# Kernel tuning notes

Hardware: AMD Instinct MI355X
Metric: run time of the kernel (lower is better)

## Reference

```python
import jax, jax.numpy as jnp
import numpy as np

B, S, H, NH = 4, 2048, 1024, 16
D = H // NH

def setup_inputs() -> dict:
    key = jax.random.key(0)
    ks = jax.random.split(key, 9)
    sc = 1.0 / np.sqrt(H)
    return {
        "x": jax.random.normal(ks[0], (B, S, H), jnp.float32),
        "Wq": jax.random.normal(ks[1], (H, H), jnp.float32) * sc,
        "bq": jax.random.normal(ks[2], (H,), jnp.float32) * 0.01,
        "Wk": jax.random.normal(ks[3], (H, H), jnp.float32) * sc,
        "bk": jax.random.normal(ks[4], (H,), jnp.float32) * 0.01,
        "Wv": jax.random.normal(ks[5], (H, H), jnp.float32) * sc,
        "bv": jax.random.normal(ks[6], (H,), jnp.float32) * 0.01,
        "Wo": jax.random.normal(ks[7], (H, H), jnp.float32) * sc,
        "bo": jax.random.normal(ks[8], (H,), jnp.float32) * 0.01,
    }

def reference(x, Wq, bq, Wk, bk, Wv, bv, Wo, bo):
    # torch Linear: y = x @ W.T + b
    def proj(x, W, b):
        # [B,S,H] -> [B,NH,S,D]
        y = jnp.einsum('bsh,oh->bso', x, W) + b
        return y.reshape(B, S, NH, D).transpose(0, 2, 1, 3)
    q = proj(x, Wq, bq)
    k = proj(x, Wk, bk)
    v = proj(x, Wv, bv)
    scores = jnp.einsum('bhqd,bhkd->bhqk', q, k) / jnp.sqrt(jnp.float32(D))
    p = jax.nn.softmax(scores, axis=-1)  # [B,NH,S,S]
    o = jnp.einsum('bhqk,bhkd->bhqd', p, v)  # dropout p=0 (eval)
    o = o.transpose(0, 2, 1, 3).reshape(B, S, H)
    return jnp.einsum('bsh,oh->bso', o, Wo) + bo
```

## Files before the change

### kernel.cpp

```cpp
#include <hip/hip_runtime.h>


#define DEV __device__ __forceinline__

typedef __bf16 bf16x8 __attribute__((ext_vector_type(8)));
typedef __bf16 bf16x4 __attribute__((ext_vector_type(4)));
typedef __bf16 bf16x2 __attribute__((ext_vector_type(2)));
typedef float floatx4 __attribute__((ext_vector_type(4)));
typedef unsigned int uintx4 __attribute__((ext_vector_type(4)));

constexpr int Bdim = 4, SS = 2048, HH = 1024, NHH = 16, DD = 64;
constexpr int MM = Bdim * SS;

DEV void async16(const void* g, void* l) {
  __builtin_amdgcn_global_load_lds(
      (const __attribute__((address_space(1))) unsigned int*)g,
      (__attribute__((address_space(3))) unsigned int*)l, 16, 0, 0);
}

DEV int swz2(int r) { return (r ^ (r >> 2)) & 3; }
DEV int swz3(int r) { return (r ^ (r >> 3)) & 7; }

DEV unsigned pkbf16(float lo, float hi) {
  bf16x2 t;
  t[0] = (__bf16)lo;
  t[1] = (__bf16)hi;
  return __builtin_bit_cast(unsigned, t);
}

DEV void pswap16(unsigned& a, unsigned& b) {
  asm("v_permlane16_swap_b32 %0, %1" : "+v"(a), "+v"(b));
}

__global__ __launch_bounds__(256) void cast_bf16_kernel(
    const float* __restrict__ x, const float* __restrict__ wq,
    const float* __restrict__ wk, const float* __restrict__ wv,
    const float* __restrict__ wo,
    __bf16* __restrict__ xb, __bf16* __restrict__ wqb, __bf16* __restrict__ wkb,
    __bf16* __restrict__ wvb, __bf16* __restrict__ wob) {
  const float* src; __bf16* dst; int n4;
  switch (blockIdx.z) {
    case 0: src = x;  dst = xb;  n4 = MM * HH / 4; break;
    case 1: src = wq; dst = wqb; n4 = HH * HH / 4; break;
    case 2: src = wk; dst = wkb; n4 = HH * HH / 4; break;
    case 3: src = wv; dst = wvb; n4 = HH * HH / 4; break;
    default: src = wo; dst = wob; n4 = HH * HH / 4; break;
  }
  int stride = gridDim.x * blockDim.x;
  for (int i = blockIdx.x * blockDim.x + threadIdx.x; i < n4; i += stride) {
    float4 v = ((const float4*)src)[i];
    bf16x4 o;
    o[0] = (__bf16)v.x; o[1] = (__bf16)v.y; o[2] = (__bf16)v.z; o[3] = (__bf16)v.w;
    ((bf16x4*)dst)[i] = o;
  }
}

__global__ __launch_bounds__(256, 3) void proj_qkv_kernel(
    const __bf16* __restrict__ xb,
    const __bf16* __restrict__ wqb, const __bf16* __restrict__ wkb,
    const __bf16* __restrict__ wvb,
    const float* __restrict__ bq, const float* __restrict__ bk,
    const float* __restrict__ bv,
    __bf16* __restrict__ Q, __bf16* __restrict__ Kc, __bf16* __restrict__ Vt) {
  __shared__ __align__(16) __bf16 As[2][128 * 32];
  __shared__ __align__(16) __bf16 Bs[2][3][64 * 32];

  const int lid = blockIdx.x;
  const int xcd = lid & 7, slot = lid >> 3;
  const int mp = xcd + 8 * (slot >> 4);
  const int np = slot & 15;
  const int m0 = mp * 128, n0 = np * 64;

  const int t = threadIdx.x;
  const int lane = t & 63, quad = lane >> 4, l16 = lane & 15;
  const int wid = t >> 6;

  const __bf16* const Wm[3] = {wqb, wkb, wvb};

  const int srow = t >> 2, sc = t & 3;
  const __bf16* Ag0 = xb + (size_t)(m0 + srow) * HH + (sc ^ swz2(srow)) * 8;
  const __bf16* Ag1 = xb + (size_t)(m0 + srow + 64) * HH + (sc ^ swz2(srow + 64)) * 8;
  const __bf16* Bg[3];
#pragma unroll
  for (int mo = 0; mo < 3; ++mo)
    Bg[mo] = Wm[mo] + (size_t)(n0 + srow) * HH + (sc ^ swz2(srow)) * 8;

  int aoff[2], boff[4];
#pragma unroll
  for (int mi = 0; mi < 2; ++mi) {
    int ra = wid * 32 + mi * 16 + l16;
    aoff[mi] = ra * 32 + (quad ^ swz2(ra)) * 8;
  }
#pragma unroll
  for (int ni = 0; ni < 4; ++ni) {
    int rb = ni * 16 + l16;
    boff[ni] = rb * 32 + (quad ^ swz2(rb)) * 8;
  }

  floatx4 acc[3][2][4] = {};

  async16(Ag0, &As[0][t * 8]);
  async16(Ag1, &As[0][2048 + t * 8]);
#pragma unroll
  for (int mo = 0; mo < 3; ++mo) async16(Bg[mo], &Bs[0][mo][t * 8]);

  for (int it = 0; it < HH / 32; ++it) {
    const int cur = it & 1;
    __syncthreads();

    if (it + 1 < HH / 32) {
      const int k = (it + 1) * 32;
      const int nxt = cur ^ 1;
      async16(Ag0 + k, &As[nxt][t * 8]);
      async16(Ag1 + k, &As[nxt][2048 + t * 8]);
#pragma unroll
      for (int mo = 0; mo < 3; ++mo) async16(Bg[mo] + k, &Bs[nxt][mo][t * 8]);
    }

    bf16x8 af[2];
#pragma unroll
    for (int mi = 0; mi < 2; ++mi) af[mi] = *(const bf16x8*)&As[cur][aoff[mi]];
#pragma unroll
    for (int mo = 0; mo < 3; ++mo) {
      bf16x8 bfr[4];
#pragma unroll
      for (int ni = 0; ni < 4; ++ni) bfr[ni] = *(const bf16x8*)&Bs[cur][mo][boff[ni]];
#pragma unroll
      for (int mi = 0; mi < 2; ++mi)
#pragma unroll
        for (int ni = 0; ni < 4; ++ni)
          acc[mo][mi][ni] = __builtin_amdgcn_mfma_f32_16x16x32_bf16(
              af[mi], bfr[ni], acc[mo][mi][ni], 0, 0, 0);
    }
  }

  const float qscale = 0.125f * 1.44269504088896f;
#pragma unroll
  for (int mo = 0; mo < 3; ++mo) {
    const float* bias = mo == 0 ? bq : mo == 1 ? bk : bv;
#pragma unroll
    for (int ni = 0; ni < 4; ++ni) {
      int n = n0 + ni * 16 + l16;
      float bval = bias[n];
      int h = n >> 6, d = n & 63;
#pragma unroll
      for (int mi = 0; mi < 2; ++mi) {
        int mbase = m0 + wid * 32 + mi * 16 + quad * 4;
        int bb = mbase >> 11, sbase = mbase & (SS - 1);
        size_t bh = (size_t)(bb * NHH + h);
        if (mo == 2) {
          bf16x4 pv;
#pragma unroll
          for (int r = 0; r < 4; ++r) pv[r] = (__bf16)(acc[mo][mi][ni][r] + bval);
          *(bf16x4*)&Vt[(bh * DD + d) * SS + sbase] = pv;
        } else {
#pragma unroll
          for (int r = 0; r < 4; ++r) {
            float v = acc[mo][mi][ni][r] + bval;
            if (mo == 0) Q [(bh * SS + sbase + r) * DD + d] = (__bf16)(v * qscale);
            else         Kc[(bh * SS + sbase + r) * DD + d] = (__bf16)v;
          }
        }
      }
    }
  }
}

DEV void gemm_db128(const __bf16* __restrict__ Ablk, const __bf16* __restrict__ Bblk,
                    __bf16* As, __bf16* Bs, floatx4 acc[4][4]) {
  const int t = threadIdx.x;
  const int lane = t & 63, quad = lane >> 4, l16 = lane & 15;
  const int wid = t >> 6;
  const int wm = (wid >> 1) * 64, wn = (wid & 1) * 64;

  const int srow = t >> 2, sc = t & 3;
  const __bf16* Ag0 = Ablk + (size_t)srow * HH + (sc ^ swz2(srow)) * 8;
  const __bf16* Ag1 = Ablk + (size_t)(srow + 64) * HH + (sc ^ swz2(srow + 64)) * 8;
  const __bf16* Bg0 = Bblk + (size_t)srow * HH + (sc ^ swz2(srow)) * 8;
  const __bf16* Bg1 = Bblk + (size_t)(srow + 64) * HH + (sc ^ swz2(srow + 64)) * 8;

  int aoff[4], boff[4];
#pragma unroll
  for (int i = 0; i < 4; ++i) {
    int ra = wm + i * 16 + l16;
    aoff[i] = ra * 32 + (quad ^ swz2(ra)) * 8;
    int rb = wn + i * 16 + l16;
    boff[i] = rb * 32 + (quad ^ swz2(rb)) * 8;
  }

  async16(Ag0, As + t * 8);
  async16(Ag1, As + 2048 + t * 8);
  async16(Bg0, Bs + t * 8);
  async16(Bg1, Bs + 2048 + t * 8);

  for (int it = 0; it < HH / 32; ++it) {
    const int cur = it & 1;
    __syncthreads();

    if (it + 1 < HH / 32) {
      const int k = (it + 1) * 32;
      const int nxt = (cur ^ 1) * 4096;
      async16(Ag0 + k, As + nxt + t * 8);
      async16(Ag1 + k, As + nxt + 2048 + t * 8);
      async16(Bg0 + k, Bs + nxt + t * 8);
      async16(Bg1 + k, Bs + nxt + 2048 + t * 8);
    }

    bf16x8 af[4], bfr[4];
#pragma unroll
    for (int i = 0; i < 4; ++i) {
      af[i]  = *(const bf16x8*)&As[cur * 4096 + aoff[i]];
      bfr[i] = *(const bf16x8*)&Bs[cur * 4096 + boff[i]];
    }
#pragma unroll
    for (int mi = 0; mi < 4; ++mi)
#pragma unroll
      for (int ni = 0; ni < 4; ++ni)
        acc[mi][ni] = __builtin_amdgcn_mfma_f32_16x16x32_bf16(af[mi], bfr[ni],
                                                              acc[mi][ni], 0, 0, 0);
  }
}

__global__ __launch_bounds__(256) void proj_out_kernel(
    const __bf16* __restrict__ Ob, const __bf16* __restrict__ wob,
    const float* __restrict__ bo, float* __restrict__ out) {
  __shared__ __align__(16) __bf16 As[2 * 128 * 32];
  __shared__ __align__(16) __bf16 Bs[2 * 128 * 32];
  const int lid = blockIdx.x;
  const int xcd = lid & 7, slot = lid >> 3;
  const int mp = xcd + 8 * (slot >> 3);
  const int np = slot & 7;
  const int m0 = mp * 128, n0 = np * 128;
  floatx4 acc[4][4] = {};
  gemm_db128(Ob + (size_t)m0 * HH, wob + (size_t)n0 * HH, As, Bs, acc);
  const int t = threadIdx.x, lane = t & 63, quad = lane >> 4, l16 = lane & 15;
  const int wid = t >> 6, wm = (wid >> 1) * 64, wn = (wid & 1) * 64;
#pragma unroll
  for (int ni = 0; ni < 4; ++ni) {
    int n = n0 + wn + ni * 16 + l16;
    float bval = bo[n];
#pragma unroll
    for (int mi = 0; mi < 4; ++mi)
#pragma unroll
      for (int r = 0; r < 4; ++r) {
        int m = m0 + wm + mi * 16 + quad * 4 + r;
        out[(size_t)m * HH + n] = acc[mi][ni][r] + bval;
      }
  }
}

__global__ __launch_bounds__(256, 2) void attn_kernel(
    const __bf16* __restrict__ Q, const __bf16* __restrict__ Kc,
    const __bf16* __restrict__ Vt, __bf16* __restrict__ Ob) {
  __shared__ __align__(16) __bf16 Ks[2][64 * 64];
  __shared__ __align__(16) __bf16 Vs[2][64 * 64];

  const int t = threadIdx.x, lane = t & 63, quad = lane >> 4, l16 = lane & 15;
  const int wid = t >> 6;
  const int L = blockIdx.x;
  const int qt = L >> 6, bhx = L & 63;
  const int b = bhx >> 4, h = bhx & 15;
  const size_t bh = (size_t)b * NHH + h;
  const __bf16* Qg = Q + (bh * SS + (size_t)qt * 256) * DD;
  const __bf16* Kg = Kc + bh * SS * DD;
  const __bf16* Vg = Vt + bh * DD * SS;

  const int srow = t >> 3;
  const int sc = t & 7;

  const __bf16* KgA = Kg + (size_t)srow * DD + (sc ^ swz3(srow)) * 8;
  const __bf16* KgB = Kg + (size_t)(srow + 32) * DD + (sc ^ swz3(srow + 32)) * 8;
  const __bf16* VgA = Vg + (size_t)srow * SS + (sc ^ swz3(srow)) * 8;
  const __bf16* VgB = Vg + (size_t)(srow + 32) * SS + (sc ^ swz3(srow + 32)) * 8;

  bf16x8 qf[4][2];
#pragma unroll
  for (int ni = 0; ni < 4; ++ni)
#pragma unroll
    for (int ks = 0; ks < 2; ++ks)
      qf[ni][ks] = *(const bf16x8*)(Qg + (size_t)(wid * 64 + ni * 16 + l16) * DD
                                    + (ks * 4 + quad) * 8);

  floatx4 oacc[4][4] = {};
  float rsum[4] = {0.f, 0.f, 0.f, 0.f};

  int koff[4][2];
#pragma unroll
  for (int mi = 0; mi < 4; ++mi) {
    int r = mi * 16 + l16;
#pragma unroll
    for (int ks = 0; ks < 2; ++ks)
      koff[mi][ks] = r * 64 + ((ks * 4 + quad) ^ swz3(r)) * 8;
  }
  const int sq = ((quad & 1) << 1) | (quad >> 1);
  int voff[4][2];
#pragma unroll
  for (int nj = 0; nj < 4; ++nj) {
    int r = nj * 16 + l16;
#pragma unroll
    for (int hf = 0; hf < 2; ++hf)
      voff[nj][hf] = r * 64 + ((hf * 4 + sq) ^ swz3(r)) * 8;
  }

  async16(KgA, &Ks[0][t * 8]);
  async16(KgB, &Ks[0][2048 + t * 8]);
  async16(VgA, &Vs[0][t * 8]);
  async16(VgB, &Vs[0][2048 + t * 8]);

  for (int kt = 0; kt < SS / 64; ++kt) {
    const int cur = kt & 1;
    __syncthreads();

    if (kt + 1 < SS / 64) {
      const int kk = (kt + 1) * 64;
      const int nxt = cur ^ 1;
      async16(KgA + (size_t)kk * DD, &Ks[nxt][t * 8]);
      async16(KgB + (size_t)kk * DD, &Ks[nxt][2048 + t * 8]);
      async16(VgA + kk, &Vs[nxt][t * 8]);
      async16(VgB + kk, &Vs[nxt][2048 + t * 8]);
    }

    floatx4 sacc[4][4];
#pragma unroll
    for (int mi = 0; mi < 4; ++mi)
#pragma unroll
      for (int ni = 0; ni < 4; ++ni) sacc[mi][ni] = floatx4{0.f, 0.f, 0.f, 0.f};
#pragma unroll
    for (int ks = 0; ks < 2; ++ks) {
      bf16x8 kf[4];
#pragma unroll
      for (int mi = 0; mi < 4; ++mi) kf[mi] = *(const bf16x8*)&Ks[cur][koff[mi][ks]];
#pragma unroll
      for (int mi = 0; mi < 4; ++mi)
#pragma unroll
        for (int ni = 0; ni < 4; ++ni)
          sacc[mi][ni] = __builtin_amdgcn_mfma_f32_16x16x32_bf16(kf[mi], qf[ni][ks],
                                                                 sacc[mi][ni], 0, 0, 0);
    }

#pragma unroll
    for (int hf = 0; hf < 2; ++hf) {
      bf16x8 ap[4], bv8[4];
#pragma unroll
      for (int mq = 0; mq < 4; ++mq) {
        float p[2][4];
#pragma unroll
        for (int m = 0; m < 2; ++m)
#pragma unroll
          for (int r = 0; r < 4; ++r) {
            float e = __builtin_amdgcn_exp2f(sacc[hf * 2 + m][mq][r]);
            rsum[mq] += e;
            p[m][r] = e;
          }
        unsigned x0 = pkbf16(p[0][0], p[0][1]);
        unsigned x1 = pkbf16(p[0][2], p[0][3]);
        unsigned y0 = pkbf16(p[1][0], p[1][1]);
        unsigned y1 = pkbf16(p[1][2], p[1][3]);
        pswap16(x0, y0);
        pswap16(x1, y1);
        uintx4 u = {x0, x1, y0, y1};
        ap[mq] = __builtin_bit_cast(bf16x8, u);
      }
#pragma unroll
      for (int nj = 0; nj < 4; ++nj) bv8[nj] = *(const bf16x8*)&Vs[cur][voff[nj][hf]];
#pragma unroll
      for (int mq = 0; mq < 4; ++mq)
#pragma unroll
        for (int nj = 0; nj < 4; ++nj)
          oacc[mq][nj] = __builtin_amdgcn_mfma_f32_16x16x32_bf16(ap[mq], bv8[nj],
                                                                 oacc[mq][nj], 0, 0, 0);
    }
  }

#pragma unroll
  for (int ni = 0; ni < 4; ++ni) {
    rsum[ni] += __shfl_xor(rsum[ni], 16, 64);
    rsum[ni] += __shfl_xor(rsum[ni], 32, 64);
  }

  const int s0 = qt * 256 + wid * 64;
#pragma unroll
  for (int mq = 0; mq < 4; ++mq) {
#pragma unroll
    for (int r = 0; r < 4; ++r) {
      float inv = 1.f / __shfl(rsum[mq], quad * 4 + r, 64);
      int s = s0 + mq * 16 + quad * 4 + r;
#pragma unroll
      for (int nj = 0; nj < 4; ++nj) {
        int d = nj * 16 + l16;
        Ob[((size_t)b * SS + s) * HH + h * DD + d] = (__bf16)(oacc[mq][nj][r] * inv);
      }
    }
  }
}

extern "C" void kernel_launch(void* const* d_in, const int* in_sizes, int n_in,
                              void* d_out, int out_size, void* d_ws, size_t ws_size,
                              hipStream_t stream) {
  const float* x  = (const float*)d_in[0];
  const float* Wq = (const float*)d_in[1];
  const float* bq = (const float*)d_in[2];
  const float* Wk = (const float*)d_in[3];
  const float* bk = (const float*)d_in[4];
  const float* Wv = (const float*)d_in[5];
  const float* bv = (const float*)d_in[6];
  const float* Wo = (const float*)d_in[7];
  const float* bo = (const float*)d_in[8];
  float* out = (float*)d_out;

  char* ws = (char*)d_ws;
  __bf16* xb  = (__bf16*)(ws);
  __bf16* wqb = (__bf16*)(ws + 16777216);
  __bf16* wkb = (__bf16*)(ws + 18874368);
  __bf16* wvb = (__bf16*)(ws + 20971520);
  __bf16* wob = (__bf16*)(ws + 23068672);
  __bf16* Qb  = (__bf16*)(ws + 25165824);
  __bf16* Kb  = (__bf16*)(ws + 41943040);
  __bf16* Vtb = (__bf16*)(ws + 58720256);
  __bf16* Ob  = (__bf16*)(ws + 75497472);

  cast_bf16_kernel<<<dim3(256, 1, 5), 256, 0, stream>>>(x, Wq, Wk, Wv, Wo,
                                                        xb, wqb, wkb, wvb, wob);
  proj_qkv_kernel<<<dim3(1024), 256, 0, stream>>>(xb, wqb, wkb, wvb,
                                                  bq, bk, bv, Qb, Kb, Vtb);
  attn_kernel<<<dim3(512), 256, 0, stream>>>(Qb, Kb, Vtb, Ob);
  proj_out_kernel<<<dim3(512), 256, 0, stream>>>(Ob, wob, bo, out);
}
```

Measured before the change: 277.6 us.

## Rewrite projection GEMMs with 128x256 tiles, 8 waves and triple-buffered K pipeline

Replaces the QKV and output projection GEMMs with a shared 8-wave routine. It uses 128x256 block tiles, K-steps of 64 staged through three LDS buffers, and split async loads interleaved with two MFMA phases under explicit barriers, waitcnts and priority hints. The QKV kernel now gives each block one of Q, K or V on a wider N tile instead of all three on a 64-wide tile, and both launches are resized to match. The goal is more reuse per LDS byte and better overlap of global loads with MFMA. The cost is much more LDS per block, fewer blocks in the grid, and fragile hand-written wait counts.

```diff
diff --git a/kernel.cpp b/kernel.cpp
--- a/kernel.cpp
+++ b/kernel.cpp
@@ -18,7 +18,6 @@
       (__attribute__((address_space(3))) unsigned int*)l, 16, 0, 0);
 }
 
-DEV int swz2(int r) { return (r ^ (r >> 2)) & 3; }
 DEV int swz3(int r) { return (r ^ (r >> 3)) & 7; }
 
 DEV unsigned pkbf16(float lo, float hi) {
@@ -55,186 +54,182 @@
   }
 }
 
-__global__ __launch_bounds__(256, 3) void proj_qkv_kernel(
+DEV void gemm8p(const __bf16* __restrict__ Ablk, const __bf16* __restrict__ Bblk,
+                __bf16* Ab, __bf16* Bb, floatx4 acc[4][4]) {
+  const int t = threadIdx.x;
+  const int lane = t & 63, quad = lane >> 4, l16 = lane & 15;
+  const int wid = t >> 6;
+  const int wm = (wid >> 2) * 64, wn = (wid & 3) * 64;
+
+  const int rl = t >> 3, ch = t & 7;
+  const __bf16* Ag[2];
+  Ag[0] = Ablk + (size_t)rl * HH + (ch ^ swz3(rl)) * 8;
+  Ag[1] = Ablk + (size_t)(rl + 64) * HH + (ch ^ swz3(rl + 64)) * 8;
+  const __bf16* Bg[4];
+#pragma unroll
+  for (int br = 0; br < 4; ++br)
+    Bg[br] = Bblk + (size_t)(rl + 64 * br) * HH + (ch ^ swz3(rl + 64 * br)) * 8;
+
+  int aoff[2][4], boff[2][4];
+#pragma unroll
+  for (int kk = 0; kk < 2; ++kk)
+#pragma unroll
+    for (int i = 0; i < 4; ++i) {
+      int ra = wm + i * 16 + l16;
+      aoff[kk][i] = ra * 64 + (((kk * 4 + quad) ^ swz3(ra)) * 8);
+      int rb = wn + i * 16 + l16;
+      boff[kk][i] = rb * 64 + (((kk * 4 + quad) ^ swz3(rb)) * 8);
+    }
+
+#pragma unroll
+  for (int tile = 0; tile < 2; ++tile) {
+    async16(Ag[0] + tile * 64, Ab + tile * 8192 + t * 8);
+    async16(Ag[1] + tile * 64, Ab + tile * 8192 + 4096 + t * 8);
+#pragma unroll
+    for (int br = 0; br < 4; ++br)
+      async16(Bg[br] + tile * 64, Bb + tile * 16384 + br * 4096 + t * 8);
+  }
+  asm volatile("s_waitcnt vmcnt(6)" ::: "memory");
+  __builtin_amdgcn_s_barrier();
+
+  int cb = 0, sb = 2;
+#pragma unroll 1
+  for (int kt = 0; kt < 16; ++kt) {
+    const __bf16* Ac = Ab + cb * 8192;
+    const __bf16* Bc = Bb + cb * 16384;
+    __bf16* Asg = Ab + sb * 8192;
+    __bf16* Bsg = Bb + sb * 16384;
+    const int ks = (kt + 2) * 64;
+    const bool st = kt < 14;
+
+    bf16x8 af[4], bfr[4];
+#pragma unroll
+    for (int i = 0; i < 4; ++i) af[i] = *(const bf16x8*)&Ac[aoff[0][i]];
+#pragma unroll
+    for (int i = 0; i < 4; ++i) bfr[i] = *(const bf16x8*)&Bc[boff[0][i]];
+    if (st) {
+      async16(Ag[0] + ks, Asg + t * 8);
+      async16(Ag[1] + ks, Asg + 4096 + t * 8);
+      async16(Bg[0] + ks, Bsg + t * 8);
+    }
+    asm volatile("" ::: "memory");
+    __builtin_amdgcn_s_barrier();
+    asm volatile("s_waitcnt lgkmcnt(0)" ::: "memory");
+    __builtin_amdgcn_sched_barrier(0);
+    __builtin_amdgcn_s_setprio(1);
+#pragma unroll
+    for (int mi = 0; mi < 4; ++mi)
+#pragma unroll
+      for (int ni = 0; ni < 4; ++ni)
+        acc[mi][ni] = __builtin_amdgcn_mfma_f32_16x16x32_bf16(af[mi], bfr[ni],
+                                                              acc[mi][ni], 0, 0, 0);
+    __builtin_amdgcn_s_setprio(0);
+    asm volatile("" ::: "memory");
+    __builtin_amdgcn_s_barrier();
+
+#pragma unroll
+    for (int i = 0; i < 4; ++i) af[i] = *(const bf16x8*)&Ac[aoff[1][i]];
+#pragma unroll
+    for (int i = 0; i < 4; ++i) bfr[i] = *(const bf16x8*)&Bc[boff[1][i]];
+    if (st) {
+      async16(Bg[1] + ks, Bsg + 4096 + t * 8);
+      async16(Bg[2] + ks, Bsg + 8192 + t * 8);
+      async16(Bg[3] + ks, Bsg + 12288 + t * 8);
+    }
+    asm volatile("" ::: "memory");
+    __builtin_amdgcn_s_barrier();
+    asm volatile("s_waitcnt lgkmcnt(0)" ::: "memory");
+    __builtin_amdgcn_sched_barrier(0);
+    __builtin_amdgcn_s_setprio(1);
+#pragma unroll
+    for (int mi = 0; mi < 4; ++mi)
+#pragma unroll
+      for (int ni = 0; ni < 4; ++ni)
+        acc[mi][ni] = __builtin_amdgcn_mfma_f32_16x16x32_bf16(af[mi], bfr[ni],
+                                                              acc[mi][ni], 0, 0, 0);
+    __builtin_amdgcn_s_setprio(0);
+    if (st) asm volatile("s_waitcnt vmcnt(6)" ::: "memory");
+    else    asm volatile("s_waitcnt vmcnt(0)" ::: "memory");
+    asm volatile("" ::: "memory");
+    __builtin_amdgcn_s_barrier();
+
+    cb = cb == 2 ? 0 : cb + 1;
+    sb = sb == 2 ? 0 : sb + 1;
+  }
+}
+
+__global__ __launch_bounds__(512, 2) void proj_qkv_kernel(
     const __bf16* __restrict__ xb,
     const __bf16* __restrict__ wqb, const __bf16* __restrict__ wkb,
     const __bf16* __restrict__ wvb,
     const float* __restrict__ bq, const float* __restrict__ bk,
     const float* __restrict__ bv,
     __bf16* __restrict__ Q, __bf16* __restrict__ Kc, __bf16* __restrict__ Vt) {
-  __shared__ __align__(16) __bf16 As[2][128 * 32];
-  __shared__ __align__(16) __bf16 Bs[2][3][64 * 32];
+  __shared__ __align__(16) __bf16 Ab[3][128 * 64];
+  __shared__ __align__(16) __bf16 Bb[3][256 * 64];
 
   const int lid = blockIdx.x;
   const int xcd = lid & 7, slot = lid >> 3;
-  const int mp = xcd + 8 * (slot >> 4);
-  const int np = slot & 15;
-  const int m0 = mp * 128, n0 = np * 64;
-
-  const int t = threadIdx.x;
-  const int lane = t & 63, quad = lane >> 4, l16 = lane & 15;
-  const int wid = t >> 6;
-
-  const __bf16* const Wm[3] = {wqb, wkb, wvb};
-
-  const int srow = t >> 2, sc = t & 3;
-  const __bf16* Ag0 = xb + (size_t)(m0 + srow) * HH + (sc ^ swz2(srow)) * 8;
-  const __bf16* Ag1 = xb + (size_t)(m0 + srow + 64) * HH + (sc ^ swz2(srow + 64)) * 8;
-  const __bf16* Bg[3];
-#pragma unroll
-  for (int mo = 0; mo < 3; ++mo)
-    Bg[mo] = Wm[mo] + (size_t)(n0 + srow) * HH + (sc ^ swz2(srow)) * 8;
-
-  int aoff[2], boff[4];
-#pragma unroll
-  for (int mi = 0; mi < 2; ++mi) {
-    int ra = wid * 32 + mi * 16 + l16;
-    aoff[mi] = ra * 32 + (quad ^ swz2(ra)) * 8;
-  }
+  const int mp = xcd + 8 * (slot & 7);
+  const int nt = slot >> 3;
+  const int mode = nt >> 2;
+  const int n0 = (nt & 3) * 256;
+  const int m0 = mp * 128;
+
+  const __bf16* W = mode == 0 ? wqb : mode == 1 ? wkb : wvb;
+  const float* bias = mode == 0 ? bq : mode == 1 ? bk : bv;
+
+  floatx4 acc[4][4] = {};
+  gemm8p(xb + (size_t)m0 * HH, W + (size_t)n0 * HH, &Ab[0][0], &Bb[0][0], acc);
+
+  const int t = threadIdx.x, lane = t & 63, quad = lane >> 4, l16 = lane & 15;
+  const int wid = t >> 6, wm = (wid >> 2) * 64, wn = (wid & 3) * 64;
+  const float qscale = 0.125f * 1.44269504088896f;
+
 #pragma unroll
   for (int ni = 0; ni < 4; ++ni) {
-    int rb = ni * 16 + l16;
-    boff[ni] = rb * 32 + (quad ^ swz2(rb)) * 8;
-  }
-
-  floatx4 acc[3][2][4] = {};
-
-  async16(Ag0, &As[0][t * 8]);
-  async16(Ag1, &As[0][2048 + t * 8]);
-#pragma unroll
-  for (int mo = 0; mo < 3; ++mo) async16(Bg[mo], &Bs[0][mo][t * 8]);
-
-  for (int it = 0; it < HH / 32; ++it) {
-    const int cur = it & 1;
-    __syncthreads();
-
-    if (it + 1 < HH / 32) {
-      const int k = (it + 1) * 32;
-      const int nxt = cur ^ 1;
-      async16(Ag0 + k, &As[nxt][t * 8]);
-      async16(Ag1 + k, &As[nxt][2048 + t * 8]);
-#pragma unroll
-      for (int mo = 0; mo < 3; ++mo) async16(Bg[mo] + k, &Bs[nxt][mo][t * 8]);
-    }
-
-    bf16x8 af[2];
-#pragma unroll
-    for (int mi = 0; mi < 2; ++mi) af[mi] = *(const bf16x8*)&As[cur][aoff[mi]];
-#pragma unroll
-    for (int mo = 0; mo < 3; ++mo) {
-      bf16x8 bfr[4];
-#pragma unroll
-      for (int ni = 0; ni < 4; ++ni) bfr[ni] = *(const bf16x8*)&Bs[cur][mo][boff[ni]];
-#pragma unroll
-      for (int mi = 0; mi < 2; ++mi)
-#pragma unroll
-        for (int ni = 0; ni < 4; ++ni)
-          acc[mo][mi][ni] = __builtin_amdgcn_mfma_f32_16x16x32_bf16(
-              af[mi], bfr[ni], acc[mo][mi][ni], 0, 0, 0);
-    }
-  }
-
-  const float qscale = 0.125f * 1.44269504088896f;
-#pragma unroll
-  for (int mo = 0; mo < 3; ++mo) {
-    const float* bias = mo == 0 ? bq : mo == 1 ? bk : bv;
-#pragma unroll
-    for (int ni = 0; ni < 4; ++ni) {
-      int n = n0 + ni * 16 + l16;
-      float bval = bias[n];
-      int h = n >> 6, d = n & 63;
-#pragma unroll
-      for (int mi = 0; mi < 2; ++mi) {
-        int mbase = m0 + wid * 32 + mi * 16 + quad * 4;
-        int bb = mbase >> 11, sbase = mbase & (SS - 1);
-        size_t bh = (size_t)(bb * NHH + h);
-        if (mo == 2) {
-          bf16x4 pv;
-#pragma unroll
-          for (int r = 0; r < 4; ++r) pv[r] = (__bf16)(acc[mo][mi][ni][r] + bval);
-          *(bf16x4*)&Vt[(bh * DD + d) * SS + sbase] = pv;
-        } else {
-#pragma unroll
-          for (int r = 0; r < 4; ++r) {
-            float v = acc[mo][mi][ni][r] + bval;
-            if (mo == 0) Q [(bh * SS + sbase + r) * DD + d] = (__bf16)(v * qscale);
-            else         Kc[(bh * SS + sbase + r) * DD + d] = (__bf16)v;
-          }
+    int n = n0 + wn + ni * 16 + l16;
+    float bval = bias[n];
+    int h = n >> 6, d = n & 63;
+#pragma unroll
+    for (int mi = 0; mi < 4; ++mi) {
+      int mbase = m0 + wm + mi * 16 + quad * 4;
+      int bb = mbase >> 11, sbase = mbase & (SS - 1);
+      size_t bh = (size_t)(bb * NHH + h);
+      if (mode == 2) {
+        bf16x4 pv;
+#pragma unroll
+        for (int r = 0; r < 4; ++r) pv[r] = (__bf16)(acc[mi][ni][r] + bval);
+        *(bf16x4*)&Vt[(bh * DD + d) * SS + sbase] = pv;
+      } else {
+#pragma unroll
+        for (int r = 0; r < 4; ++r) {
+          float v = acc[mi][ni][r] + bval;
+          if (mode == 0) Q [(bh * SS + sbase + r) * DD + d] = (__bf16)(v * qscale);
+          else           Kc[(bh * SS + sbase + r) * DD + d] = (__bf16)v;
         }
       }
     }
   }
 }
 
-DEV void gemm_db128(const __bf16* __restrict__ Ablk, const __bf16* __restrict__ Bblk,
-                    __bf16* As, __bf16* Bs, floatx4 acc[4][4]) {
-  const int t = threadIdx.x;
-  const int lane = t & 63, quad = lane >> 4, l16 = lane & 15;
-  const int wid = t >> 6;
-  const int wm = (wid >> 1) * 64, wn = (wid & 1) * 64;
-
-  const int srow = t >> 2, sc = t & 3;
-  const __bf16* Ag0 = Ablk + (size_t)srow * HH + (sc ^ swz2(srow)) * 8;
-  const __bf16* Ag1 = Ablk + (size_t)(srow + 64) * HH + (sc ^ swz2(srow + 64)) * 8;
-  const __bf16* Bg0 = Bblk + (size_t)srow * HH + (sc ^ swz2(srow)) * 8;
-  const __bf16* Bg1 = Bblk + (size_t)(srow + 64) * HH + (sc ^ swz2(srow + 64)) * 8;
-
-  int aoff[4], boff[4];
-#pragma unroll
-  for (int i = 0; i < 4; ++i) {
-    int ra = wm + i * 16 + l16;
-    aoff[i] = ra * 32 + (quad ^ swz2(ra)) * 8;
-    int rb = wn + i * 16 + l16;
-    boff[i] = rb * 32 + (quad ^ swz2(rb)) * 8;
-  }
-
-  async16(Ag0, As + t * 8);
-  async16(Ag1, As + 2048 + t * 8);
-  async16(Bg0, Bs + t * 8);
-  async16(Bg1, Bs + 2048 + t * 8);
-
-  for (int it = 0; it < HH / 32; ++it) {
-    const int cur = it & 1;
-    __syncthreads();
-
-    if (it + 1 < HH / 32) {
-      const int k = (it + 1) * 32;
-      const int nxt = (cur ^ 1) * 4096;
-      async16(Ag0 + k, As + nxt + t * 8);
-      async16(Ag1 + k, As + nxt + 2048 + t * 8);
-      async16(Bg0 + k, Bs + nxt + t * 8);
-      async16(Bg1 + k, Bs + nxt + 2048 + t * 8);
-    }
-
-    bf16x8 af[4], bfr[4];
-#pragma unroll
-    for (int i = 0; i < 4; ++i) {
-      af[i]  = *(const bf16x8*)&As[cur * 4096 + aoff[i]];
-      bfr[i] = *(const bf16x8*)&Bs[cur * 4096 + boff[i]];
-    }
-#pragma unroll
-    for (int mi = 0; mi < 4; ++mi)
-#pragma unroll
-      for (int ni = 0; ni < 4; ++ni)
-        acc[mi][ni] = __builtin_amdgcn_mfma_f32_16x16x32_bf16(af[mi], bfr[ni],
-                                                              acc[mi][ni], 0, 0, 0);
-  }
-}
-
-__global__ __launch_bounds__(256) void proj_out_kernel(
+__global__ __launch_bounds__(512, 2) void proj_out_kernel(
     const __bf16* __restrict__ Ob, const __bf16* __restrict__ wob,
     const float* __restrict__ bo, float* __restrict__ out) {
-  __shared__ __align__(16) __bf16 As[2 * 128 * 32];
-  __shared__ __align__(16) __bf16 Bs[2 * 128 * 32];
+  __shared__ __align__(16) __bf16 Ab[3][128 * 64];
+  __shared__ __align__(16) __bf16 Bb[3][256 * 64];
+
   const int lid = blockIdx.x;
   const int xcd = lid & 7, slot = lid >> 3;
-  const int mp = xcd + 8 * (slot >> 3);
-  const int np = slot & 7;
-  const int m0 = mp * 128, n0 = np * 128;
+  const int mp = xcd + 8 * (slot & 7);
+  const int np = slot >> 3;
+  const int m0 = mp * 128, n0 = np * 256;
+
   floatx4 acc[4][4] = {};
-  gemm_db128(Ob + (size_t)m0 * HH, wob + (size_t)n0 * HH, As, Bs, acc);
+  gemm8p(Ob + (size_t)m0 * HH, wob + (size_t)n0 * HH, &Ab[0][0], &Bb[0][0], acc);
+
   const int t = threadIdx.x, lane = t & 63, quad = lane >> 4, l16 = lane & 15;
-  const int wid = t >> 6, wm = (wid >> 1) * 64, wn = (wid & 1) * 64;
+  const int wid = t >> 6, wm = (wid >> 2) * 64, wn = (wid & 3) * 64;
 #pragma unroll
   for (int ni = 0; ni < 4; ++ni) {
     int n = n0 + wn + ni * 16 + l16;
@@ -421,8 +416,8 @@
 
   cast_bf16_kernel<<<dim3(256, 1, 5), 256, 0, stream>>>(x, Wq, Wk, Wv, Wo,
                                                         xb, wqb, wkb, wvb, wob);
-  proj_qkv_kernel<<<dim3(1024), 256, 0, stream>>>(xb, wqb, wkb, wvb,
-                                                  bq, bk, bv, Qb, Kb, Vtb);
+  proj_qkv_kernel<<<dim3(768), 512, 0, stream>>>(xb, wqb, wkb, wvb,
+                                                 bq, bk, bv, Qb, Kb, Vtb);
   attn_kernel<<<dim3(512), 256, 0, stream>>>(Qb, Kb, Vtb, Ob);
-  proj_out_kernel<<<dim3(512), 256, 0, stream>>>(Ob, wob, bo, out);
-}
+  proj_out_kernel<<<dim3(256), 512, 0, stream>>>(Ob, wob, bo, out);
+}
```

Measured after the change: 268.5 us. 3.3% less time.
